# Performance work log

Hardware: AMD Instinct MI355X
Metric: run time of the kernel (lower is better)

Reference implementation:

```python
import jax, jax.numpy as jnp
import numpy as np

B, S, E, H = 2, 2048, 2048, 16
D = E // H  # head_dim = 128


def setup_inputs() -> dict:
    key = jax.random.key(0)
    ks = jax.random.split(key, 11)
    scale = 1.0 / np.sqrt(E)
    return {
        "query": jax.random.normal(ks[0], (B, S, E), dtype=jnp.float32),
        "key_in": jax.random.normal(ks[1], (B, S, E), dtype=jnp.float32),
        "value": jax.random.normal(ks[2], (B, S, E), dtype=jnp.float32),
        "Wq": jax.random.normal(ks[3], (E, E), dtype=jnp.float32) * scale,
        "bq": jnp.zeros((E,), dtype=jnp.float32),
        "Wk": jax.random.normal(ks[4], (E, E), dtype=jnp.float32) * scale,
        "bk": jnp.zeros((E,), dtype=jnp.float32),
        "Wv": jax.random.normal(ks[5], (E, E), dtype=jnp.float32) * scale,
        "bv": jnp.zeros((E,), dtype=jnp.float32),
        "Wo": jax.random.normal(ks[6], (E, E), dtype=jnp.float32) * scale,
        "bo": jnp.zeros((E,), dtype=jnp.float32),
    }


def reference(query, key_in, value, Wq, bq, Wk, bk, Wv, bv, Wo, bo):
    # Linear projections then split heads: (B,S,E) -> (B,H,S,D)
    def proj(x, W, b):
        y = x @ W + b
        return y.reshape(B, S, H, D).transpose(0, 2, 1, 3)

    Q = proj(query, Wq, bq)
    K = proj(key_in, Wk, bk)
    V = proj(value, Wv, bv)

    # scores: (B,H,S,S)
    scores = jnp.einsum('bhqd,bhkd->bhqk', Q, K) / jnp.sqrt(jnp.float32(D))
    attn = jax.nn.softmax(scores, axis=-1)
    # attn output: (B,H,S,D) -> (B,S,E)
    out = jnp.einsum('bhqk,bhkd->bhqd', attn, V)
    out = out.transpose(0, 2, 1, 3).reshape(B, S, E)
    return out @ Wo + bo
```

## Files before the change

### kernel.cpp

```cpp
#include <hip/hip_runtime.h>
#include <hip/hip_bf16.h>

typedef __bf16 bf16;
typedef __bf16 bf16x8 __attribute__((ext_vector_type(8)));
typedef float f32x4 __attribute__((ext_vector_type(4)));

constexpr int kE = 2048;
constexpr int kS = 2048;
constexpr int kB = 2;
constexpr int kH = 16;
constexpr int kD = 128;
constexpr int kM = kB * kS;
constexpr float kQScale = 0.12751743f;

#define MFMA_BF16(A, B, C) __builtin_amdgcn_mfma_f32_16x16x32_bf16((A), (B), (C), 0, 0, 0)

__device__ __forceinline__ void async_ld16(const void* gsrc, void* ldst) {
  __builtin_amdgcn_global_load_lds(
      (__attribute__((address_space(1))) void*)(gsrc),
      (__attribute__((address_space(3))) void*)(ldst), 16, 0, 0);
}

__global__ __launch_bounds__(256) void cvt_kernel(
    const float* __restrict__ Xq, const float* __restrict__ Xk,
    const float* __restrict__ Xv, bf16* __restrict__ Y) {
  const int z = blockIdx.y;
  const float* X = (z == 0) ? Xq : (z == 1) ? Xk : Xv;
  bf16* Yz = Y + (size_t)z * kM * kE;
  size_t i = ((size_t)blockIdx.x * 256 + threadIdx.x) * 8;
  float4 v0 = *(const float4*)(X + i);
  float4 v1 = *(const float4*)(X + i + 4);
  bf16x8 hv;
  hv[0] = (bf16)v0.x; hv[1] = (bf16)v0.y; hv[2] = (bf16)v0.z; hv[3] = (bf16)v0.w;
  hv[4] = (bf16)v1.x; hv[5] = (bf16)v1.y; hv[6] = (bf16)v1.z; hv[7] = (bf16)v1.w;
  *(bf16x8*)(Yz + i) = hv;
}

__global__ __launch_bounds__(256) void wt_kernel(
    const float* __restrict__ Wq, const float* __restrict__ Wk,
    const float* __restrict__ Wv, const float* __restrict__ Wo,
    bf16* __restrict__ WT) {
  __shared__ bf16 tl[64][72];
  const int z = blockIdx.z;
  const float* W = (z == 0) ? Wq : (z == 1) ? Wk : (z == 2) ? Wv : Wo;
  const int n0 = blockIdx.x * 64, k0 = blockIdx.y * 64;
  const int t = threadIdx.x;

  {
    const int k = t >> 2, nq = (t & 3) * 16;
    const float* src = &W[(size_t)(k0 + k) * kE + n0 + nq];
#pragma unroll
    for (int u = 0; u < 4; ++u) {
      float4 v = *(const float4*)(src + u * 4);
      tl[nq + u * 4 + 0][k] = (bf16)v.x;
      tl[nq + u * 4 + 1][k] = (bf16)v.y;
      tl[nq + u * 4 + 2][k] = (bf16)v.z;
      tl[nq + u * 4 + 3][k] = (bf16)v.w;
    }
  }
  __syncthreads();
  {
    const int n = t >> 2, seg = (t & 3) * 16;
    bf16x8 a = *(const bf16x8*)&tl[n][seg];
    bf16x8 b2 = *(const bf16x8*)&tl[n][seg + 8];
    bf16* dst = &WT[(size_t)(z * kE + n0 + n) * kE + k0 + seg];
    *(bf16x8*)dst = a;
    *(bf16x8*)(dst + 8) = b2;
  }
}

__global__ __launch_bounds__(256) void gemm_qkv_kernel(
    const bf16* __restrict__ A, const bf16* __restrict__ Bt,
    const float* __restrict__ bias, bf16* __restrict__ dstbuf,
    const float oscale) {
  __shared__ alignas(16) bf16 As[128 * 64];
  __shared__ alignas(16) bf16 Bs[128 * 64];

  const int n0 = blockIdx.x * 128;
  const int m0 = blockIdx.y * 128;
  const int t = threadIdx.x;
  const int lane = t & 63;
  const int w = t >> 6;
  const int ln = lane & 15;
  const int qd = lane >> 4;
  const int wm = w >> 1, wn = w & 1;

  const f32x4 fzero = {0.f, 0.f, 0.f, 0.f};
  f32x4 acc[4][4];
#pragma unroll
  for (int i = 0; i < 4; ++i)
#pragma unroll
    for (int j = 0; j < 4; ++j) acc[i][j] = fzero;

  for (int k0 = 0; k0 < kE; k0 += 64) {
    __syncthreads();
#pragma unroll
    for (int i = 0; i < 4; ++i) {
      int c = t + i * 256;
      int row = c >> 3;
      int slot = c & 7;
      int g = slot ^ (row & 7);
      async_ld16(&A[(size_t)(m0 + row) * kE + k0 + g * 8],
                 &As[(size_t)(w * 64 + i * 256) * 8]);
    }
#pragma unroll
    for (int i = 0; i < 4; ++i) {
      int c = t + i * 256;
      int row = c >> 3;
      int slot = c & 7;
      int g = slot ^ (row & 7);
      async_ld16(&Bt[(size_t)(n0 + row) * kE + k0 + g * 8],
                 &Bs[(size_t)(w * 64 + i * 256) * 8]);
    }
    __syncthreads();
#pragma unroll
    for (int ks = 0; ks < 2; ++ks) {
      bf16x8 af[4], bfv[4];
#pragma unroll
      for (int i = 0; i < 4; ++i) {
        int row = wm * 64 + i * 16 + ln;
        int slot = (ks * 4 + qd) ^ (ln & 7);
        af[i] = *(const bf16x8*)&As[row * 64 + slot * 8];
      }
#pragma unroll
      for (int j = 0; j < 4; ++j) {
        int row = wn * 64 + j * 16 + ln;
        int slot = (ks * 4 + qd) ^ (ln & 7);
        bfv[j] = *(const bf16x8*)&Bs[row * 64 + slot * 8];
      }
#pragma unroll
      for (int i = 0; i < 4; ++i)
#pragma unroll
        for (int j = 0; j < 4; ++j)
          acc[i][j] = MFMA_BF16(af[i], bfv[j], acc[i][j]);
    }
  }

#pragma unroll
  for (int i = 0; i < 4; ++i) {
    int mbase = m0 + wm * 64 + i * 16 + qd * 4;
#pragma unroll
    for (int j = 0; j < 4; ++j) {
      int n = n0 + wn * 64 + j * 16 + ln;
      float bn = bias[n];
      int h = n >> 7, d = n & 127;
#pragma unroll
      for (int r = 0; r < 4; ++r) {
        int mm = mbase + r;
        int bb = mm >> 11, ss = mm & (kS - 1);
        dstbuf[((size_t)(bb * kH + h) * kS + ss) * kD + d] =
            (bf16)((acc[i][j][r] + bn) * oscale);
      }
    }
  }
}

__global__ __launch_bounds__(256) void vtrans_kernel(
    const bf16* __restrict__ Vb, bf16* __restrict__ VT) {
  __shared__ bf16 tl[64][72];
  const int bh = blockIdx.z;
  const int s0 = blockIdx.x * 64, d0 = blockIdx.y * 64;
  const bf16* src = Vb + ((size_t)bh * kS + s0) * kD + d0;
  bf16* dst = VT + ((size_t)bh * kD + d0) * kS + s0;
  const int t = threadIdx.x;
#pragma unroll
  for (int i = 0; i < 2; ++i) {
    int c = t + i * 256;
    int s = c >> 3, dc = (c & 7) * 8;
    bf16x8 v = *(const bf16x8*)&src[(size_t)s * kD + dc];
#pragma unroll
    for (int e = 0; e < 8; ++e) tl[dc + e][s] = v[e];
  }
  __syncthreads();
#pragma unroll
  for (int i = 0; i < 2; ++i) {
    int c = t + i * 256;
    int d = c >> 3, sc = (c & 7) * 8;
    bf16x8 v = *(const bf16x8*)&tl[d][sc];
    *(bf16x8*)&dst[(size_t)d * kS + sc] = v;
  }
}

__global__ __launch_bounds__(256) void attn_kernel(
    const bf16* __restrict__ Qb, const bf16* __restrict__ Kb,
    const bf16* __restrict__ VTb, bf16* __restrict__ AO) {
  __shared__ alignas(16) bf16 Kt[64 * 128];
  __shared__ alignas(16) bf16 Vt[128 * 64];
  __shared__ alignas(16) bf16 Pl[4][32 * 64];

  const int b = blockIdx.z, h = blockIdx.y;
  const int q0 = blockIdx.x * 128;
  const int t = threadIdx.x, lane = t & 63, w = t >> 6;
  const int ln = lane & 15, qd = lane >> 4;

  const bf16* Qh = Qb + (size_t)(b * kH + h) * kS * kD;
  const bf16* Kh = Kb + (size_t)(b * kH + h) * kS * kD;
  const bf16* Vh = VTb + (size_t)(b * kH + h) * kD * kS;

  bf16x8 qf[2][4];
#pragma unroll
  for (int m = 0; m < 2; ++m) {
    int qr = q0 + w * 32 + m * 16 + ln;
#pragma unroll
    for (int f = 0; f < 4; ++f)
      qf[m][f] = *(const bf16x8*)&Qh[(size_t)qr * kD + f * 32 + qd * 8];
  }

  const f32x4 fzero = {0.f, 0.f, 0.f, 0.f};
  f32x4 o[2][8];
#pragma unroll
  for (int m = 0; m < 2; ++m)
#pragma unroll
    for (int dt = 0; dt < 8; ++dt) o[m][dt] = fzero;
  float lsum[2][4] = {{0.f, 0.f, 0.f, 0.f}, {0.f, 0.f, 0.f, 0.f}};

  for (int kc = 0; kc < kS; kc += 64) {
    __syncthreads();
#pragma unroll
    for (int i = 0; i < 4; ++i) {
      int c = t + i * 256;
      int row = c >> 4;
      int slot = c & 15;
      int g = slot ^ (row & 15);
      async_ld16(&Kh[(size_t)(kc + row) * kD + g * 8],
                 &Kt[(size_t)(w * 64 + i * 256) * 8]);
    }
#pragma unroll
    for (int i = 0; i < 4; ++i) {
      int c = t + i * 256;
      int row = c >> 3;
      int slot = c & 7;
      int g = slot ^ (row & 7);
      async_ld16(&Vh[(size_t)row * kS + kc + g * 8],
                 &Vt[(size_t)(w * 64 + i * 256) * 8]);
    }
    __syncthreads();

    f32x4 s[2][4];
#pragma unroll
    for (int m = 0; m < 2; ++m)
#pragma unroll
      for (int nt = 0; nt < 4; ++nt) s[m][nt] = fzero;
#pragma unroll
    for (int nt = 0; nt < 4; ++nt) {
      int row = nt * 16 + ln;
#pragma unroll
      for (int f = 0; f < 4; ++f) {
        int slot = (f * 4 + qd) ^ ln;
        bf16x8 kfv = *(const bf16x8*)&Kt[row * 128 + slot * 8];
        s[0][nt] = MFMA_BF16(qf[0][f], kfv, s[0][nt]);
        s[1][nt] = MFMA_BF16(qf[1][f], kfv, s[1][nt]);
      }
    }

#pragma unroll
    for (int m = 0; m < 2; ++m)
#pragma unroll
      for (int nt = 0; nt < 4; ++nt)
#pragma unroll
        for (int r = 0; r < 4; ++r) {
          float p = __builtin_amdgcn_exp2f(s[m][nt][r]);
          lsum[m][r] += p;
          int prow = m * 16 + qd * 4 + r;
          int gchunk = nt * 2 + (ln >> 3);
          int slot = gchunk ^ (prow & 7);
          Pl[w][prow * 64 + slot * 8 + (ln & 7)] = (bf16)p;
        }
    asm volatile("s_waitcnt lgkmcnt(0)" ::: "memory");

    bf16x8 pf[2][2];
#pragma unroll
    for (int m = 0; m < 2; ++m)
#pragma unroll
      for (int kf = 0; kf < 2; ++kf) {
        int slot = (kf * 4 + qd) ^ (ln & 7);
        pf[m][kf] = *(const bf16x8*)&Pl[w][(m * 16 + ln) * 64 + slot * 8];
      }
#pragma unroll
    for (int dt = 0; dt < 8; ++dt) {
      int row = dt * 16 + ln;
#pragma unroll
      for (int kf = 0; kf < 2; ++kf) {
        int slot = (kf * 4 + qd) ^ (ln & 7);
        bf16x8 vv = *(const bf16x8*)&Vt[row * 64 + slot * 8];
        o[0][dt] = MFMA_BF16(pf[0][kf], vv, o[0][dt]);
        o[1][dt] = MFMA_BF16(pf[1][kf], vv, o[1][dt]);
      }
    }
  }

#pragma unroll
  for (int m = 0; m < 2; ++m)
#pragma unroll
    for (int r = 0; r < 4; ++r) {
      float l = lsum[m][r];
      l += __shfl_xor(l, 1);
      l += __shfl_xor(l, 2);
      l += __shfl_xor(l, 4);
      l += __shfl_xor(l, 8);
      float inv = 1.f / l;
      int srow = q0 + w * 32 + m * 16 + qd * 4 + r;
      bf16* dst = AO + (size_t)(b * kS + srow) * kE + h * kD;
#pragma unroll
      for (int dt = 0; dt < 8; ++dt)
        dst[dt * 16 + ln] = (bf16)(o[m][dt][r] * inv);
    }
}

__global__ __launch_bounds__(256) void gemm_out_kernel(
    const bf16* __restrict__ A, const bf16* __restrict__ Bt,
    const float* __restrict__ bias, float* __restrict__ out) {
  __shared__ alignas(16) bf16 As[128 * 64];
  __shared__ alignas(16) bf16 Bs[128 * 64];

  const int n0 = blockIdx.x * 128;
  const int m0 = blockIdx.y * 128;
  const int t = threadIdx.x;
  const int lane = t & 63;
  const int w = t >> 6;
  const int ln = lane & 15;
  const int qd = lane >> 4;
  const int wm = w >> 1, wn = w & 1;

  const f32x4 fzero = {0.f, 0.f, 0.f, 0.f};
  f32x4 acc[4][4];
#pragma unroll
  for (int i = 0; i < 4; ++i)
#pragma unroll
    for (int j = 0; j < 4; ++j) acc[i][j] = fzero;

  for (int k0 = 0; k0 < kE; k0 += 64) {
    __syncthreads();
#pragma unroll
    for (int i = 0; i < 4; ++i) {
      int c = t + i * 256;
      int row = c >> 3;
      int slot = c & 7;
      int g = slot ^ (row & 7);
      async_ld16(&A[(size_t)(m0 + row) * kE + k0 + g * 8],
                 &As[(size_t)(w * 64 + i * 256) * 8]);
    }
#pragma unroll
    for (int i = 0; i < 4; ++i) {
      int c = t + i * 256;
      int row = c >> 3;
      int slot = c & 7;
      int g = slot ^ (row & 7);
      async_ld16(&Bt[(size_t)(n0 + row) * kE + k0 + g * 8],
                 &Bs[(size_t)(w * 64 + i * 256) * 8]);
    }
    __syncthreads();
#pragma unroll
    for (int ks = 0; ks < 2; ++ks) {
      bf16x8 af[4], bfv[4];
#pragma unroll
      for (int i = 0; i < 4; ++i) {
        int row = wm * 64 + i * 16 + ln;
        int slot = (ks * 4 + qd) ^ (ln & 7);
        af[i] = *(const bf16x8*)&As[row * 64 + slot * 8];
      }
#pragma unroll
      for (int j = 0; j < 4; ++j) {
        int row = wn * 64 + j * 16 + ln;
        int slot = (ks * 4 + qd) ^ (ln & 7);
        bfv[j] = *(const bf16x8*)&Bs[row * 64 + slot * 8];
      }
#pragma unroll
      for (int i = 0; i < 4; ++i)
#pragma unroll
        for (int j = 0; j < 4; ++j)
          acc[i][j] = MFMA_BF16(af[i], bfv[j], acc[i][j]);
    }
  }

#pragma unroll
  for (int i = 0; i < 4; ++i) {
    int mbase = m0 + wm * 64 + i * 16 + qd * 4;
#pragma unroll
    for (int j = 0; j < 4; ++j) {
      int n = n0 + wn * 64 + j * 16 + ln;
      float bn = bias[n];
#pragma unroll
      for (int r = 0; r < 4; ++r) {
        int mm = mbase + r;
        out[(size_t)mm * kE + n] = acc[i][j][r] + bn;
      }
    }
  }
}

extern "C" void kernel_launch(void* const* d_in, const int* in_sizes, int n_in,
                              void* d_out, int out_size, void* d_ws,
                              size_t ws_size, hipStream_t stream) {
  const float* query  = (const float*)d_in[0];
  const float* key_in = (const float*)d_in[1];
  const float* value  = (const float*)d_in[2];
  const float* Wq = (const float*)d_in[3];
  const float* bq = (const float*)d_in[4];
  const float* Wk = (const float*)d_in[5];
  const float* bk = (const float*)d_in[6];
  const float* Wv = (const float*)d_in[7];
  const float* bv = (const float*)d_in[8];
  const float* Wo = (const float*)d_in[9];
  const float* bo = (const float*)d_in[10];
  float* out = (float*)d_out;

  const size_t szWT  = (size_t)4 * kE * kE;
  const size_t szAct = (size_t)kM * kE;
  const size_t need = (szWT + 7 * szAct) * sizeof(bf16);
  if (ws_size < need) return;

  bf16* WT  = (bf16*)d_ws;
  bf16* Qb  = WT + szWT;
  bf16* Kb  = Qb + szAct;
  bf16* VTb = Kb + szAct;
  bf16* AO  = VTb + szAct;
  bf16* Xb  = AO + szAct;
  bf16* Vb  = AO;

  wt_kernel<<<dim3(kE / 64, kE / 64, 4), 256, 0, stream>>>(
      Wq, Wk, Wv, Wo, WT);
  cvt_kernel<<<dim3(kM * kE / 8 / 256, 3), 256, 0, stream>>>(
      query, key_in, value, Xb);
  gemm_qkv_kernel<<<dim3(kE / 128, kM / 128), 256, 0, stream>>>(
      Xb, WT, bq, Qb, kQScale);
  gemm_qkv_kernel<<<dim3(kE / 128, kM / 128), 256, 0, stream>>>(
      Xb + szAct, WT + (size_t)kE * kE, bk, Kb, 1.0f);
  gemm_qkv_kernel<<<dim3(kE / 128, kM / 128), 256, 0, stream>>>(
      Xb + 2 * szAct, WT + (size_t)2 * kE * kE, bv, Vb, 1.0f);
  vtrans_kernel<<<dim3(kS / 64, kD / 64, kB * kH), 256, 0, stream>>>(
      Vb, VTb);
  attn_kernel<<<dim3(kS / 128, kH, kB), 256, 0, stream>>>(Qb, Kb, VTb, AO);
  gemm_out_kernel<<<dim3(kE / 128, kM / 128), 256, 0, stream>>>(
      AO, WT + (size_t)3 * kE * kE, bo, out);
}
```

Before: 518.5 us.

## Double-buffer K/V tiles in attention and swizzle workgroups across XCDs

The attention kernel now double-buffers K and V tiles in LDS, issuing async loads for the next chunk before computing on the current one, so global latency overlaps the MFMA work. The launch becomes a 1D grid with a swizzle that maps consecutive workgroups of the same head onto the same XCD, aiming for better L2 reuse of K/V. It also raises wave priority around the MFMA blocks. In exchange LDS use doubles, which may lower occupancy, and the final iteration issues a redundant reload.

Measured after the change: 461.9 us. -10.9%, faster.

```diff
diff --git a/kernel.cpp b/kernel.cpp
--- a/kernel.cpp
+++ b/kernel.cpp
@@ -184,18 +184,20 @@
 __global__ __launch_bounds__(256) void attn_kernel(
     const bf16* __restrict__ Qb, const bf16* __restrict__ Kb,
     const bf16* __restrict__ VTb, bf16* __restrict__ AO) {
-  __shared__ alignas(16) bf16 Kt[64 * 128];
-  __shared__ alignas(16) bf16 Vt[128 * 64];
+  __shared__ alignas(16) bf16 Kt[2][64 * 128];
+  __shared__ alignas(16) bf16 Vt[2][128 * 64];
   __shared__ alignas(16) bf16 Pl[4][32 * 64];
 
-  const int b = blockIdx.z, h = blockIdx.y;
-  const int q0 = blockIdx.x * 128;
+  const int wg = blockIdx.x;
+  const int swz = (wg & 7) * 64 + (wg >> 3);
+  const int bh = swz >> 4;
+  const int q0 = (swz & 15) * 128;
   const int t = threadIdx.x, lane = t & 63, w = t >> 6;
   const int ln = lane & 15, qd = lane >> 4;
 
-  const bf16* Qh = Qb + (size_t)(b * kH + h) * kS * kD;
-  const bf16* Kh = Kb + (size_t)(b * kH + h) * kS * kD;
-  const bf16* Vh = VTb + (size_t)(b * kH + h) * kD * kS;
+  const bf16* Qh = Qb + (size_t)bh * kS * kD;
+  const bf16* Kh = Kb + (size_t)bh * kS * kD;
+  const bf16* Vh = VTb + (size_t)bh * kD * kS;
 
   bf16x8 qf[2][4];
 #pragma unroll
@@ -206,16 +208,7 @@
       qf[m][f] = *(const bf16x8*)&Qh[(size_t)qr * kD + f * 32 + qd * 8];
   }
 
-  const f32x4 fzero = {0.f, 0.f, 0.f, 0.f};
-  f32x4 o[2][8];
-#pragma unroll
-  for (int m = 0; m < 2; ++m)
-#pragma unroll
-    for (int dt = 0; dt < 8; ++dt) o[m][dt] = fzero;
-  float lsum[2][4] = {{0.f, 0.f, 0.f, 0.f}, {0.f, 0.f, 0.f, 0.f}};
-
-  for (int kc = 0; kc < kS; kc += 64) {
-    __syncthreads();
+  auto stage = [&](int buf, int kc) {
 #pragma unroll
     for (int i = 0; i < 4; ++i) {
       int c = t + i * 256;
@@ -223,7 +216,7 @@
       int slot = c & 15;
       int g = slot ^ (row & 15);
       async_ld16(&Kh[(size_t)(kc + row) * kD + g * 8],
-                 &Kt[(size_t)(w * 64 + i * 256) * 8]);
+                 &Kt[buf][(size_t)(w * 64 + i * 256) * 8]);
     }
 #pragma unroll
     for (int i = 0; i < 4; ++i) {
@@ -232,26 +225,47 @@
       int slot = c & 7;
       int g = slot ^ (row & 7);
       async_ld16(&Vh[(size_t)row * kS + kc + g * 8],
-                 &Vt[(size_t)(w * 64 + i * 256) * 8]);
-    }
-    __syncthreads();
+                 &Vt[buf][(size_t)(w * 64 + i * 256) * 8]);
+    }
+  };
+
+  const f32x4 fzero = {0.f, 0.f, 0.f, 0.f};
+  f32x4 o[2][8];
+#pragma unroll
+  for (int m = 0; m < 2; ++m)
+#pragma unroll
+    for (int dt = 0; dt < 8; ++dt) o[m][dt] = fzero;
+  float lsum[2][4] = {{0.f, 0.f, 0.f, 0.f}, {0.f, 0.f, 0.f, 0.f}};
+
+  stage(0, 0);
+
+#pragma unroll 1
+  for (int u = 0; u < 32; ++u) {
+    const int cur = u & 1;
+    int knext = (u < 31) ? (u + 1) * 64 : 31 * 64;
+    stage(cur ^ 1, knext);
+    asm volatile("s_waitcnt vmcnt(8)" ::: "memory");
+    __builtin_amdgcn_s_barrier();
+    asm volatile("" ::: "memory");
 
     f32x4 s[2][4];
 #pragma unroll
     for (int m = 0; m < 2; ++m)
 #pragma unroll
       for (int nt = 0; nt < 4; ++nt) s[m][nt] = fzero;
+    __builtin_amdgcn_s_setprio(1);
 #pragma unroll
     for (int nt = 0; nt < 4; ++nt) {
       int row = nt * 16 + ln;
 #pragma unroll
       for (int f = 0; f < 4; ++f) {
         int slot = (f * 4 + qd) ^ ln;
-        bf16x8 kfv = *(const bf16x8*)&Kt[row * 128 + slot * 8];
+        bf16x8 kfv = *(const bf16x8*)&Kt[cur][row * 128 + slot * 8];
         s[0][nt] = MFMA_BF16(qf[0][f], kfv, s[0][nt]);
         s[1][nt] = MFMA_BF16(qf[1][f], kfv, s[1][nt]);
       }
     }
+    __builtin_amdgcn_s_setprio(0);
 
 #pragma unroll
     for (int m = 0; m < 2; ++m)
@@ -276,17 +290,23 @@
         int slot = (kf * 4 + qd) ^ (ln & 7);
         pf[m][kf] = *(const bf16x8*)&Pl[w][(m * 16 + ln) * 64 + slot * 8];
       }
+    __builtin_amdgcn_s_setprio(1);
 #pragma unroll
     for (int dt = 0; dt < 8; ++dt) {
       int row = dt * 16 + ln;
 #pragma unroll
       for (int kf = 0; kf < 2; ++kf) {
         int slot = (kf * 4 + qd) ^ (ln & 7);
-        bf16x8 vv = *(const bf16x8*)&Vt[row * 64 + slot * 8];
+        bf16x8 vv = *(const bf16x8*)&Vt[cur][row * 64 + slot * 8];
         o[0][dt] = MFMA_BF16(pf[0][kf], vv, o[0][dt]);
         o[1][dt] = MFMA_BF16(pf[1][kf], vv, o[1][dt]);
       }
     }
+    __builtin_amdgcn_s_setprio(0);
+
+    asm volatile("s_waitcnt lgkmcnt(0)" ::: "memory");
+    __builtin_amdgcn_s_barrier();
+    asm volatile("" ::: "memory");
   }
 
 #pragma unroll
@@ -300,7 +320,7 @@
       l += __shfl_xor(l, 8);
       float inv = 1.f / l;
       int srow = q0 + w * 32 + m * 16 + qd * 4 + r;
-      bf16* dst = AO + (size_t)(b * kS + srow) * kE + h * kD;
+      bf16* dst = AO + (size_t)((bh >> 4) * kS + srow) * kE + (bh & 15) * kD;
 #pragma unroll
       for (int dt = 0; dt < 8; ++dt)
         dst[dt * 16 + ln] = (bf16)(o[m][dt][r] * inv);
@@ -430,7 +450,7 @@
       Xb + 2 * szAct, WT + (size_t)2 * kE * kE, bv, Vb, 1.0f);
   vtrans_kernel<<<dim3(kS / 64, kD / 64, kB * kH), 256, 0, stream>>>(
       Vb, VTb);
-  attn_kernel<<<dim3(kS / 128, kH, kB), 256, 0, stream>>>(Qb, Kb, VTb, AO);
+  attn_kernel<<<dim3(kS * kB * kH / 128), 256, 0, stream>>>(Qb, Kb, VTb, AO);
   gemm_out_kernel<<<dim3(kE / 128, kM / 128), 256, 0, stream>>>(
       AO, WT + (size_t)3 * kE * kE, bo, out);
 }
```
